# Optimization experiments

Hardware: AMD Instinct MI355X
Metric: run time of the kernel (lower is better)

## Reference

```python
import jax, jax.numpy as jnp
import numpy as np

N, IN_DIM, HID_DIM, N_CLASSES, MLP_W = 4096, 256, 128, 2, 16


def setup_inputs() -> dict:
    key = jax.random.key(0)
    ks = jax.random.split(key, 8)
    u = jax.random.uniform(ks[0], (N, N), dtype=jnp.float32)
    adj = jnp.where(u < 0.01, 1.0, 0.0).astype(jnp.float32)
    deg_row = adj.sum(axis=1)  # [N]
    deg_col = adj.sum(axis=0)  # [N]
    # per-edge row/col degree features, materialized NxN as in the source
    xdeg = (jnp.broadcast_to(deg_row[:, None], (N, N)) * jnp.ones((1,), jnp.float32)).astype(jnp.float32)
    ydeg = (jnp.broadcast_to(deg_col[None, :], (N, N)) * jnp.ones((1,), jnp.float32)).astype(jnp.float32)
    x = jax.random.normal(ks[1], (N, IN_DIM), dtype=jnp.float32)
    s = 0.1
    We1 = jax.random.normal(ks[2], (3, MLP_W), dtype=jnp.float32) * s
    be1 = jnp.zeros((MLP_W,), jnp.float32)
    We2 = jax.random.normal(ks[3], (MLP_W, 2), dtype=jnp.float32) * s
    be2 = jnp.zeros((2,), jnp.float32)
    W1 = jax.random.normal(ks[4], (IN_DIM, HID_DIM), dtype=jnp.float32) * s
    b1 = jnp.zeros((HID_DIM,), jnp.float32)
    W2 = jax.random.normal(ks[5], (HID_DIM, N_CLASSES), dtype=jnp.float32) * s
    b2 = jnp.zeros((N_CLASSES,), jnp.float32)
    resid_weight = jnp.array(0.5, dtype=jnp.float32)  # learned scalar (init 0.0 in source)
    return {"x": x, "adj": adj, "xdeg": xdeg, "ydeg": ydeg,
            "We1": We1, "be1": be1, "We2": We2, "be2": be2,
            "W1": W1, "b1": b1, "W2": W2, "b2": b2,
            "resid_weight": resid_weight}


def reference(x, adj, xdeg, ydeg, We1, be1, We2, be2, W1, b1, W2, b2, resid_weight):
    n = adj.shape[0]
    # Edge-gating MLP over (adj, xdeg, ydeg). The source gathers nonzero entries,
    # runs the MLP, and scatters back into a zero tensor; computing densely and
    # masking by (adj != 0) is mathematically identical (adj * gate kills zeros).
    feats = jnp.stack([adj, xdeg, ydeg], axis=-1)            # [N, N, 3]
    h = jax.nn.relu(jnp.einsum('nmf,fw->nmw', feats, We1) + be1)  # [N, N, 16]
    gate = jax.nn.softmax(jnp.einsum('nmw,wc->nmc', h, We2) + be2, axis=-1)[..., 1]
    gate = jnp.where(adj != 0.0, gate, 0.0)
    A = adj * gate + jnp.eye(n, dtype=adj.dtype)             # reweighted + self-loops
    # Degree normalization: source does A @ D_col, transpose, @ D_row, transpose,
    # which equals drow[:,None] * A * dcol[None,:]; use broadcasting (no O(N^3) diag mm).
    rs = A.sum(axis=1)
    cs = A.sum(axis=0)
    drow = jnp.where(rs > 0, rs ** -0.5, 0.0)
    dcol = jnp.where(cs > 0, cs ** -0.5, 0.0)
    An = drow[:, None] * A * dcol[None, :]
    # Layer 1: propagate, residual, linear (nn1 = MLP([in, hid]) -> single Linear).
    out = An @ x + resid_weight * x
    hid = out @ W1 + b1
    # dropout is identity in eval mode
    # Layer 2: propagate, residual, classifier.
    out2 = An @ hid + resid_weight * hid
    return out2 @ W2 + b2
```

## Files before the change

kernel.cpp:

```cpp
#include <hip/hip_runtime.h>


typedef unsigned char u8;

#define N_NODES 4096
#define MAX_DEG 128
#define LUTD    128

__global__ __launch_bounds__(256)
void k_prep(const float* __restrict__ We1, const float* __restrict__ be1,
            const float* __restrict__ We2, const float* __restrict__ be2,
            const float* __restrict__ W1,  const float* __restrict__ b1,
            const float* __restrict__ W2,  const float* __restrict__ b2,
            const float* __restrict__ ydeg,
            float* __restrict__ lut, float* __restrict__ M,
            float* __restrict__ cz, float* __restrict__ cfin,
            u8* __restrict__ dc_u8, float* __restrict__ cs) {
    int b = blockIdx.x, tid = threadIdx.x;
    if (b < 64) {
        int e = b * 256 + tid;
        float dr = (float)(e >> 7), dc = (float)(e & 127);
        float delta = be2[1] - be2[0];
        #pragma unroll
        for (int w = 0; w < 16; ++w) {
            float hh = fmaf(We1[32 + w], dc,
                       fmaf(We1[16 + w], dr, We1[w] + be1[w]));
            hh = fmaxf(hh, 0.f);
            delta = fmaf(hh, We2[w * 2 + 1] - We2[w * 2], delta);
        }
        lut[e] = 1.f / (1.f + __expf(-delta));
    } else if (b < 66) {
        int e = (b - 64) * 256 + tid;
        int t = e >> 1, d = e & 1;
        float s = 0.f;
        for (int h = 0; h < 128; ++h)
            s = fmaf(W1[t * 128 + h], W2[h * 2 + d], s);
        M[e] = s;
    } else if (b == 66) {
        if (tid < 2) {
            float s = 0.f;
            for (int h = 0; h < 128; ++h)
                s = fmaf(b1[h], W2[h * 2 + tid], s);
            cz[tid]   = s;
            cfin[tid] = b2[tid];
        }
    } else {
        int j = (b - 67) * 256 + tid;
        int d = (int)ydeg[j];
        dc_u8[j] = (u8)(d > 127 ? 127 : d);
        cs[j] = 0.f;
    }
}

__global__ __launch_bounds__(256)
void k_gatey(const float* __restrict__ adj, const float* __restrict__ xdeg,
             const float* __restrict__ x, const float* __restrict__ lut,
             const u8* __restrict__ dc_u8, const float* __restrict__ M,
             int2* __restrict__ e_g, float* __restrict__ rs,
             float* __restrict__ cs, int* __restrict__ cnt,
             float* __restrict__ y) {
    __shared__ float g_row[LUTD];
    __shared__ int   s_cnt;
    __shared__ float s_rs[4], s_y0[4], s_y1[4];
    const int i = blockIdx.x, tid = threadIdx.x;
    const int wv = tid >> 6, lane = tid & 63;
    if (tid == 0) s_cnt = 0;
    if (tid < LUTD) {
        int dri = (int)xdeg[(size_t)i * N_NODES];
        if (dri > 127) dri = 127;
        g_row[tid] = lut[dri * LUTD + tid];
    }
    float xv = x[(size_t)i * 256 + tid];
    float p0 = xv * M[tid * 2], p1 = xv * M[tid * 2 + 1];
    #pragma unroll
    for (int o = 32; o > 0; o >>= 1) {
        p0 += __shfl_down(p0, o);
        p1 += __shfl_down(p1, o);
    }
    if (lane == 0) { s_y0[wv] = p0; s_y1[wv] = p1; }
    __syncthreads();

    const float* arow = adj + (size_t)i * N_NODES;
    int2* er = e_g + (size_t)i * MAX_DEG;
    float lrs = 0.f;
    #pragma unroll
    for (int c = 0; c < 4; ++c) {
        int j0 = c * 1024 + tid * 4;
        float4 v = *reinterpret_cast<const float4*>(arow + j0);
        float vals[4] = {v.x, v.y, v.z, v.w};
        #pragma unroll
        for (int q = 0; q < 4; ++q) {
            if (vals[q] != 0.f) {
                int j = j0 + q;
                float gate = g_row[dc_u8[j]];
                lrs += gate;
                atomicAdd(cs + j, gate);
                int pos = atomicAdd(&s_cnt, 1);
                if (pos < MAX_DEG) er[pos] = make_int2(j, __float_as_int(gate));
            }
        }
    }
    #pragma unroll
    for (int o = 32; o > 0; o >>= 1) lrs += __shfl_down(lrs, o);
    if (lane == 0) s_rs[wv] = lrs;
    __syncthreads();
    if (tid == 0) {
        rs[i]  = 1.f + s_rs[0] + s_rs[1] + s_rs[2] + s_rs[3];
        cnt[i] = (s_cnt < MAX_DEG) ? s_cnt : MAX_DEG;
        y[i * 2 + 0] = s_y0[0] + s_y0[1] + s_y0[2] + s_y0[3];
        y[i * 2 + 1] = s_y1[0] + s_y1[1] + s_y1[2] + s_y1[3];
    }
}

__global__ __launch_bounds__(256)
void k_spmv(const int2* __restrict__ e_g, const int* __restrict__ cnt,
            const float* __restrict__ rs, const float* __restrict__ cs,
            const float* __restrict__ vin, const float* __restrict__ addv,
            const float* __restrict__ rw, float* __restrict__ vout) {
    int wv = threadIdx.x >> 6, lane = threadIdx.x & 63;
    int i = blockIdx.x * 4 + wv;
    int nnz = cnt[i];
    const int2* ep = e_g + (size_t)i * MAX_DEG;
    float a0 = 0.f, a1 = 0.f;
    for (int k = lane; k < nnz; k += 64) {
        int2 e = ep[k];
        int j = e.x;
        float wt = __int_as_float(e.y) * rsqrtf(cs[j] + 1.f);
        a0 = fmaf(wt, vin[j * 2 + 0], a0);
        a1 = fmaf(wt, vin[j * 2 + 1], a1);
    }
    #pragma unroll
    for (int o = 32; o > 0; o >>= 1) {
        a0 += __shfl_down(a0, o);
        a1 += __shfl_down(a1, o);
    }
    if (lane == 0) {
        float r  = rw[0];
        float di = rsqrtf(rs[i]), ci = rsqrtf(cs[i] + 1.f);
        float y0 = vin[i * 2 + 0], y1 = vin[i * 2 + 1];
        vout[i * 2 + 0] = di * (a0 + ci * y0) + r * y0 + addv[0];
        vout[i * 2 + 1] = di * (a1 + ci * y1) + r * y1 + addv[1];
    }
}

extern "C" void kernel_launch(void* const* d_in, const int* in_sizes, int n_in,
                              void* d_out, int out_size, void* d_ws, size_t ws_size,
                              hipStream_t stream) {
    const float* x    = (const float*)d_in[0];
    const float* adj  = (const float*)d_in[1];
    const float* xdeg = (const float*)d_in[2];
    const float* ydeg = (const float*)d_in[3];
    const float* We1  = (const float*)d_in[4];
    const float* be1  = (const float*)d_in[5];
    const float* We2  = (const float*)d_in[6];
    const float* be2  = (const float*)d_in[7];
    const float* W1   = (const float*)d_in[8];
    const float* b1   = (const float*)d_in[9];
    const float* W2   = (const float*)d_in[10];
    const float* b2   = (const float*)d_in[11];
    const float* rw   = (const float*)d_in[12];

    char* ws = (char*)d_ws;
    int2*  e_g  = (int2*) (ws + 0);
    float* lut  = (float*)(ws + 4194304);
    float* rs   = (float*)(ws + 4259840);
    float* cs   = (float*)(ws + 4276224);
    int*   cnt  = (int*)  (ws + 4292608);
    float* y    = (float*)(ws + 4308992);
    float* z    = (float*)(ws + 4341760);
    float* M    = (float*)(ws + 4374528);
    float* cz   = (float*)(ws + 4376576);
    float* cfin = (float*)(ws + 4376584);
    u8*    dcu  = (u8*)   (ws + 4376592);

    k_prep<<<83, 256, 0, stream>>>(We1, be1, We2, be2, W1, b1, W2, b2, ydeg,
                                   lut, M, cz, cfin, dcu, cs);
    k_gatey<<<N_NODES, 256, 0, stream>>>(adj, xdeg, x, lut, dcu, M,
                                         e_g, rs, cs, cnt, y);
    k_spmv<<<N_NODES / 4, 256, 0, stream>>>(e_g, cnt, rs, cs, y, cz, rw, z);
    k_spmv<<<N_NODES / 4, 256, 0, stream>>>(e_g, cnt, rs, cs, z, cfin, rw, (float*)d_out);
}
```

Baseline: 209.7 us.

## Process one adjacency row per wavefront with ballot-based edge compaction

The gate/compaction kernel now gives each wavefront its own row instead of each block. It preloads all 16 float4 chunks of the row into registers and replaces the shared-memory atomic counter with ballot/popcount prefix positions, which removes block-level syncs and LDS atomics. The SpMV kernel moves to 32-lane groups per row with float2 loads, since rows have only about 41 nonzeros. Edge order in the compacted list becomes deterministic. The change trades this for more registers per thread (64 floats for the row chunks).

```diff
diff --git a/kernel.cpp b/kernel.cpp
--- a/kernel.cpp
+++ b/kernel.cpp
@@ -59,56 +59,59 @@
              int2* __restrict__ e_g, float* __restrict__ rs,
              float* __restrict__ cs, int* __restrict__ cnt,
              float* __restrict__ y) {
-    __shared__ float g_row[LUTD];
-    __shared__ int   s_cnt;
-    __shared__ float s_rs[4], s_y0[4], s_y1[4];
-    const int i = blockIdx.x, tid = threadIdx.x;
-    const int wv = tid >> 6, lane = tid & 63;
-    if (tid == 0) s_cnt = 0;
-    if (tid < LUTD) {
-        int dri = (int)xdeg[(size_t)i * N_NODES];
-        if (dri > 127) dri = 127;
-        g_row[tid] = lut[dri * LUTD + tid];
-    }
-    float xv = x[(size_t)i * 256 + tid];
-    float p0 = xv * M[tid * 2], p1 = xv * M[tid * 2 + 1];
+    __shared__ float g_row[4][LUTD];
+    const int wv = threadIdx.x >> 6, lane = threadIdx.x & 63;
+    const int i = blockIdx.x * 4 + wv;
+
+    int dri = (int)xdeg[(size_t)i * N_NODES];
+    if (dri > 127) dri = 127;
+    float2 g2 = ((const float2*)(lut + dri * LUTD))[lane];
+    g_row[wv][lane * 2 + 0] = g2.x;
+    g_row[wv][lane * 2 + 1] = g2.y;
+
+    float4 xv = ((const float4*)(x + (size_t)i * 256))[lane];
+    float4 m01 = ((const float4*)M)[lane * 2 + 0];
+    float4 m23 = ((const float4*)M)[lane * 2 + 1];
+    float p0 = xv.x * m01.x + xv.y * m01.z + xv.z * m23.x + xv.w * m23.z;
+    float p1 = xv.x * m01.y + xv.y * m01.w + xv.z * m23.y + xv.w * m23.w;
+
+    const float4* arow4 = (const float4*)(adj + (size_t)i * N_NODES);
+    float4 v[16];
     #pragma unroll
-    for (int o = 32; o > 0; o >>= 1) {
-        p0 += __shfl_down(p0, o);
-        p1 += __shfl_down(p1, o);
-    }
-    if (lane == 0) { s_y0[wv] = p0; s_y1[wv] = p1; }
-    __syncthreads();
+    for (int c = 0; c < 16; ++c) v[c] = arow4[lane + 64 * c];
 
-    const float* arow = adj + (size_t)i * N_NODES;
     int2* er = e_g + (size_t)i * MAX_DEG;
+    int base = 0;
     float lrs = 0.f;
+    const unsigned long long lt_mask = (1ull << lane) - 1ull;
     #pragma unroll
-    for (int c = 0; c < 4; ++c) {
-        int j0 = c * 1024 + tid * 4;
-        float4 v = *reinterpret_cast<const float4*>(arow + j0);
-        float vals[4] = {v.x, v.y, v.z, v.w};
+    for (int c = 0; c < 16; ++c) {
+        float vals[4] = {v[c].x, v[c].y, v[c].z, v[c].w};
         #pragma unroll
         for (int q = 0; q < 4; ++q) {
-            if (vals[q] != 0.f) {
-                int j = j0 + q;
-                float gate = g_row[dc_u8[j]];
+            bool nz = (vals[q] != 0.f);
+            unsigned long long mask = __ballot(nz);
+            if (nz) {
+                int j = c * 256 + lane * 4 + q;
+                float gate = g_row[wv][dc_u8[j]];
                 lrs += gate;
                 atomicAdd(cs + j, gate);
-                int pos = atomicAdd(&s_cnt, 1);
+                int pos = base + __popcll(mask & lt_mask);
                 if (pos < MAX_DEG) er[pos] = make_int2(j, __float_as_int(gate));
             }
+            base += __popcll(mask);
         }
     }
     #pragma unroll
-    for (int o = 32; o > 0; o >>= 1) lrs += __shfl_down(lrs, o);
-    if (lane == 0) s_rs[wv] = lrs;
-    __syncthreads();
-    if (tid == 0) {
-        rs[i]  = 1.f + s_rs[0] + s_rs[1] + s_rs[2] + s_rs[3];
-        cnt[i] = (s_cnt < MAX_DEG) ? s_cnt : MAX_DEG;
-        y[i * 2 + 0] = s_y0[0] + s_y0[1] + s_y0[2] + s_y0[3];
-        y[i * 2 + 1] = s_y1[0] + s_y1[1] + s_y1[2] + s_y1[3];
+    for (int o = 32; o > 0; o >>= 1) {
+        lrs += __shfl_down(lrs, o);
+        p0  += __shfl_down(p0, o);
+        p1  += __shfl_down(p1, o);
+    }
+    if (lane == 0) {
+        rs[i]  = 1.f + lrs;
+        cnt[i] = (base < MAX_DEG) ? base : MAX_DEG;
+        ((float2*)y)[i] = make_float2(p0, p1);
     }
 }
 
@@ -117,29 +120,31 @@
             const float* __restrict__ rs, const float* __restrict__ cs,
             const float* __restrict__ vin, const float* __restrict__ addv,
             const float* __restrict__ rw, float* __restrict__ vout) {
-    int wv = threadIdx.x >> 6, lane = threadIdx.x & 63;
-    int i = blockIdx.x * 4 + wv;
+    int sub = threadIdx.x >> 5, lane32 = threadIdx.x & 31;
+    int i = blockIdx.x * 8 + sub;
     int nnz = cnt[i];
     const int2* ep = e_g + (size_t)i * MAX_DEG;
     float a0 = 0.f, a1 = 0.f;
-    for (int k = lane; k < nnz; k += 64) {
+    for (int k = lane32; k < nnz; k += 32) {
         int2 e = ep[k];
-        int j = e.x;
-        float wt = __int_as_float(e.y) * rsqrtf(cs[j] + 1.f);
-        a0 = fmaf(wt, vin[j * 2 + 0], a0);
-        a1 = fmaf(wt, vin[j * 2 + 1], a1);
+        float2 vj = ((const float2*)vin)[e.x];
+        float wt = __int_as_float(e.y) * rsqrtf(cs[e.x] + 1.f);
+        a0 = fmaf(wt, vj.x, a0);
+        a1 = fmaf(wt, vj.y, a1);
     }
     #pragma unroll
-    for (int o = 32; o > 0; o >>= 1) {
-        a0 += __shfl_down(a0, o);
-        a1 += __shfl_down(a1, o);
+    for (int o = 16; o > 0; o >>= 1) {
+        a0 += __shfl_down(a0, o, 32);
+        a1 += __shfl_down(a1, o, 32);
     }
-    if (lane == 0) {
+    if (lane32 == 0) {
         float r  = rw[0];
         float di = rsqrtf(rs[i]), ci = rsqrtf(cs[i] + 1.f);
-        float y0 = vin[i * 2 + 0], y1 = vin[i * 2 + 1];
-        vout[i * 2 + 0] = di * (a0 + ci * y0) + r * y0 + addv[0];
-        vout[i * 2 + 1] = di * (a1 + ci * y1) + r * y1 + addv[1];
+        float2 yv = ((const float2*)vin)[i];
+        float2 o;
+        o.x = di * (a0 + ci * yv.x) + r * yv.x + addv[0];
+        o.y = di * (a1 + ci * yv.y) + r * yv.y + addv[1];
+        ((float2*)vout)[i] = o;
     }
 }
 
@@ -175,8 +180,8 @@
 
     k_prep<<<83, 256, 0, stream>>>(We1, be1, We2, be2, W1, b1, W2, b2, ydeg,
                                    lut, M, cz, cfin, dcu, cs);
-    k_gatey<<<N_NODES, 256, 0, stream>>>(adj, xdeg, x, lut, dcu, M,
-                                         e_g, rs, cs, cnt, y);
-    k_spmv<<<N_NODES / 4, 256, 0, stream>>>(e_g, cnt, rs, cs, y, cz, rw, z);
-    k_spmv<<<N_NODES / 4, 256, 0, stream>>>(e_g, cnt, rs, cs, z, cfin, rw, (float*)d_out);
+    k_gatey<<<N_NODES / 4, 256, 0, stream>>>(adj, xdeg, x, lut, dcu, M,
+                                             e_g, rs, cs, cnt, y);
+    k_spmv<<<N_NODES / 8, 256, 0, stream>>>(e_g, cnt, rs, cs, y, cz, rw, z);
+    k_spmv<<<N_NODES / 8, 256, 0, stream>>>(e_g, cnt, rs, cs, z, cfin, rw, (float*)d_out);
 }
```

After: 238.7 us. 1.14x slower.
